# Kernel tuning notes

Hardware: AMD Instinct MI355X
Metric: run time of the kernel (lower is better)

Reference implementation:

```python
import jax, jax.numpy as jnp
import numpy as np

HID = 16
DATA_DIM = 2
B = 2048
T = 64
RTOL, ATOL = 1e-2, 1e-4
SAFETY, FMIN, FMAX = 0.9, 0.2, 10.0
MAX_STEPS = 16  # bounded adaptive-step budget (masked once t reaches T1)
T1 = 1.0
DT0 = 1.0

# Tsit5 (Tsitouras 2011) tableau
_A2 = (0.161,)
_A3 = (-0.008480655492356989, 0.335480655492357)
_A4 = (2.8971530571054935, -6.359448489975075, 4.3622954328695815)
_A5 = (5.325864828439257, -11.748883564062828, 7.4955393428898365, -0.09249506636175525)
_A6 = (5.86145544294642, -12.92096931784711, 8.159367898576159, -0.071584973281401, -0.028269050394068383)
_B5 = (0.09646076681806523, 0.01, 0.4798896504144996, 1.379008574103742, -3.290069515436081, 2.324710524099774)
_BT = (-0.00178001105222577714, -0.0008164344596567469, 0.007880878010261995, -0.1447110071732629, 0.5823571654525552, -0.45808210592918697, 0.015151515151515152)


def setup_inputs() -> dict:
    key = jax.random.key(0)
    ks = jax.random.split(key, 13)
    u = lambda k, shape, fan: jax.random.uniform(k, shape, jnp.float32, -1.0, 1.0) / np.float32(np.sqrt(fan))
    return dict(
        x_seq=jax.random.normal(ks[0], (B, T, DATA_DIM), jnp.float32),
        w1=u(ks[1], (HID, HID), HID), b1=u(ks[2], (HID,), HID),
        w2=u(ks[3], (HID, HID), HID), b2=u(ks[4], (HID,), HID),
        w3=u(ks[5], (HID, HID), HID), b3=u(ks[6], (HID,), HID),
        gru_wih=u(ks[7], (3 * HID, DATA_DIM), DATA_DIM),
        gru_whh=u(ks[8], (3 * HID, HID), HID),
        gru_b=u(ks[9], (3 * HID,), HID),
        gru_bn=u(ks[10], (HID,), HID),
        pred_w=u(ks[11], (1, HID), HID),
        pred_b=u(ks[12], (1,), HID),
    )


def _mlp(y, w1, b1, w2, b2, w3, b3):
    # eqx.nn.MLP(in=16, out=16, width=16, depth=2, activation=tanh): 3 Linear layers
    y = jnp.tanh(y @ w1.T + b1)
    y = jnp.tanh(y @ w2.T + b2)
    return y @ w3.T + b3


def _ode_solve(h0, f):
    """Adaptive Tsit5 + I-controller (diffrax PIDController defaults) from t=0 to t=1.
    Per-sample adaptive step/accept/reject, batched over the leading axis."""
    nB = h0.shape[0]

    def body(state, _):
        y, t, dt = state                      # y:[B,16]  t,dt:[B]
        dt_c = jnp.minimum(dt, T1 - t)        # clip so we never overshoot t1
        d = dt_c[:, None]
        k1 = f(y)
        k2 = f(y + d * (_A2[0] * k1))
        k3 = f(y + d * (_A3[0] * k1 + _A3[1] * k2))
        k4 = f(y + d * (_A4[0] * k1 + _A4[1] * k2 + _A4[2] * k3))
        k5 = f(y + d * (_A5[0] * k1 + _A5[1] * k2 + _A5[2] * k3 + _A5[3] * k4))
        k6 = f(y + d * (_A6[0] * k1 + _A6[1] * k2 + _A6[2] * k3 + _A6[3] * k4 + _A6[4] * k5))
        y_new = y + d * (_B5[0] * k1 + _B5[1] * k2 + _B5[2] * k3 + _B5[3] * k4 + _B5[4] * k5 + _B5[5] * k6)
        k7 = f(y_new)                          # FSAL stage, enters only the error estimate
        err = d * (_BT[0] * k1 + _BT[1] * k2 + _BT[2] * k3 + _BT[3] * k4 + _BT[4] * k5 + _BT[5] * k6 + _BT[6] * k7)
        scale = ATOL + RTOL * jnp.maximum(jnp.abs(y), jnp.abs(y_new))
        err2 = jnp.maximum(jnp.mean((err / scale) ** 2, axis=-1), 1e-16)  # squared RMS norm, [B]
        accept = err2 <= 1.0
        y = jnp.where(accept[:, None], y_new, y)
        t = jnp.where(accept, t + dt_c, t)
        # I-controller: factor = safety * err_norm**(-1/order), order=5
        factor = jnp.clip(SAFETY * err2 ** (-0.1), FMIN, FMAX)
        dt = dt_c * factor
        return (y, t, dt), None

    init = (h0, jnp.zeros((nB,), h0.dtype), jnp.full((nB,), DT0, h0.dtype))
    (y, _, _), _ = jax.lax.scan(body, init, None, length=MAX_STEPS)
    return y


def _gru(x, h, wih, whh, b, bn):
    # eqx.nn.GRUCell math
    ig = x @ wih.T + b
    hg = h @ whh.T
    ir, iz, inn = jnp.split(ig, 3, axis=-1)
    hr, hz, hn = jnp.split(hg, 3, axis=-1)
    r = jax.nn.sigmoid(ir + hr)
    z = jax.nn.sigmoid(iz + hz)
    n = jnp.tanh(inn + r * (hn + bn))
    return n + z * (h - n)


def reference(x_seq, w1, b1, w2, b2, w3, b3, gru_wih, gru_whh, gru_b, gru_bn, pred_w, pred_b):
    f = lambda y: _mlp(y, w1, b1, w2, b2, w3, b3)
    h0 = jnp.zeros((x_seq.shape[0], HID), x_seq.dtype)

    def step(h, x_t):
        h_ev = _ode_solve(h, f)
        h_new = _gru(x_t, h_ev, gru_wih, gru_whh, gru_b, gru_bn)
        return h_new, None

    xs = jnp.swapaxes(x_seq, 0, 1)  # [T, B, D]
    h_final, _ = jax.lax.scan(step, h0, xs)
    return h_final @ pred_w.T + pred_b  # [B, 1]
```

## Files before the change

### kernel.cpp

```cpp
#include <hip/hip_runtime.h>


#define T_STEPS 64
#define NB 2048
#define N_ODE_STEPS 16

#define ROR(x, r) __int_as_float(__builtin_amdgcn_update_dpp( \
    0, __float_as_int(x), 0x120 + (r), 0xF, 0xF, true))

__device__ __forceinline__ float rsum16(float v) {
  v += ROR(v, 8);
  v += ROR(v, 4);
  v += ROR(v, 2);
  v += ROR(v, 1);
  return v;
}

__device__ __forceinline__ float dot16(const float (&w)[16], float y) {
  float a0 = w[0] * y;
  float a1 = w[1] * ROR(y, 1);
  float a2 = w[2] * ROR(y, 2);
  float a3 = w[3] * ROR(y, 3);
  a0 = fmaf(w[4],  ROR(y, 4),  a0);
  a1 = fmaf(w[5],  ROR(y, 5),  a1);
  a2 = fmaf(w[6],  ROR(y, 6),  a2);
  a3 = fmaf(w[7],  ROR(y, 7),  a3);
  a0 = fmaf(w[8],  ROR(y, 8),  a0);
  a1 = fmaf(w[9],  ROR(y, 9),  a1);
  a2 = fmaf(w[10], ROR(y, 10), a2);
  a3 = fmaf(w[11], ROR(y, 11), a3);
  a0 = fmaf(w[12], ROR(y, 12), a0);
  a1 = fmaf(w[13], ROR(y, 13), a1);
  a2 = fmaf(w[14], ROR(y, 14), a2);
  a3 = fmaf(w[15], ROR(y, 15), a3);
  return (a0 + a1) + (a2 + a3);
}

__device__ __forceinline__ float fast_tanh(float x) {
  float e = __builtin_amdgcn_exp2f(x * 2.885390081777927f);
  return fmaf(-2.0f, __builtin_amdgcn_rcpf(e + 1.0f), 1.0f);
}

__device__ __forceinline__ float sigmoid_(float x) {
  float e = __builtin_amdgcn_exp2f(x * -1.4426950408889634f);
  return __builtin_amdgcn_rcpf(1.0f + e);
}

__device__ __forceinline__ float mlp_f(float y,
    const float (&w1r)[16], float b1v,
    const float (&w2r)[16], float b2v,
    const float (&w3r)[16], float b3v) {
  float h1 = fast_tanh(dot16(w1r, y) + b1v);
  float h2 = fast_tanh(dot16(w2r, h1) + b2v);
  return dot16(w3r, h2) + b3v;
}

__global__ __launch_bounds__(64, 1) void odern_kernel(
    const float* __restrict__ x_seq,
    const float* __restrict__ w1, const float* __restrict__ b1,
    const float* __restrict__ w2, const float* __restrict__ b2,
    const float* __restrict__ w3, const float* __restrict__ b3,
    const float* __restrict__ gru_wih, const float* __restrict__ gru_whh,
    const float* __restrict__ gru_b, const float* __restrict__ gru_bn,
    const float* __restrict__ pred_w, const float* __restrict__ pred_b,
    float* __restrict__ out) {
  const int tid = threadIdx.x;
  const int j = tid & 15;
  const int g = tid >> 4;
  const int b = blockIdx.x * 4 + g;

  float w1r[16], w2r[16], w3r[16], whr[16], wzr[16], wnr[16];
#pragma unroll
  for (int r = 0; r < 16; ++r) {
    const int i = (j - r) & 15;
    w1r[r] = w1[j * 16 + i];
    w2r[r] = w2[j * 16 + i];
    w3r[r] = w3[j * 16 + i];
    whr[r] = gru_whh[j * 16 + i];
    wzr[r] = gru_whh[(16 + j) * 16 + i];
    wnr[r] = gru_whh[(32 + j) * 16 + i];
  }
  const float b1v = b1[j], b2v = b2[j], b3v = b3[j];
  const float wih_r0 = gru_wih[j * 2],        wih_r1 = gru_wih[j * 2 + 1];
  const float wih_z0 = gru_wih[(16 + j) * 2], wih_z1 = gru_wih[(16 + j) * 2 + 1];
  const float wih_n0 = gru_wih[(32 + j) * 2], wih_n1 = gru_wih[(32 + j) * 2 + 1];
  const float gb_r = gru_b[j], gb_z = gru_b[16 + j], gb_n = gru_b[32 + j];
  const float bnv = gru_bn[j];
  const float pwv = pred_w[j], pbv = pred_b[0];

  const float* xp = x_seq + (size_t)b * (T_STEPS * 2);

  float h = 0.0f;
#pragma unroll 1
  for (int t = 0; t < T_STEPS; ++t) {
    const float x0 = xp[2 * t];
    const float x1 = xp[2 * t + 1];

    float y = h;
    float tt = 0.0f, dt = 1.0f;
    float k1 = mlp_f(y, w1r, b1v, w2r, b2v, w3r, b3v);
#pragma unroll 1
    for (int s = 0; s < N_ODE_STEPS; ++s) {
      if (__all(tt >= 1.0f)) break;

      const float dt_c = fminf(dt, 1.0f - tt);
      const float d = dt_c;

      float s2 = 0.161f * k1;
      float k2 = mlp_f(fmaf(d, s2, y), w1r, b1v, w2r, b2v, w3r, b3v);

      float s3 = fmaf(0.335480655492357f, k2, -0.008480655492356989f * k1);
      float k3 = mlp_f(fmaf(d, s3, y), w1r, b1v, w2r, b2v, w3r, b3v);

      float s4 = fmaf(4.3622954328695815f, k3,
                 fmaf(-6.359448489975075f, k2, 2.8971530571054935f * k1));
      float k4 = mlp_f(fmaf(d, s4, y), w1r, b1v, w2r, b2v, w3r, b3v);

      float s5 = fmaf(-0.09249506636175525f, k4,
                 fmaf(7.4955393428898365f, k3,
                 fmaf(-11.748883564062828f, k2, 5.325864828439257f * k1)));
      float k5 = mlp_f(fmaf(d, s5, y), w1r, b1v, w2r, b2v, w3r, b3v);

      float s6 = fmaf(-0.028269050394068383f, k5,
                 fmaf(-0.071584973281401f, k4,
                 fmaf(8.159367898576159f, k3,
                 fmaf(-12.92096931784711f, k2, 5.86145544294642f * k1))));
      float k6 = mlp_f(fmaf(d, s6, y), w1r, b1v, w2r, b2v, w3r, b3v);

      float sy = fmaf(2.324710524099774f, k6,
                 fmaf(-3.290069515436081f, k5,
                 fmaf(1.379008574103742f, k4,
                 fmaf(0.4798896504144996f, k3,
                 fmaf(0.01f, k2, 0.09646076681806523f * k1)))));
      float y_new = fmaf(d, sy, y);

      float k7 = mlp_f(y_new, w1r, b1v, w2r, b2v, w3r, b3v);

      float se = fmaf(0.015151515151515152f, k7,
                 fmaf(-0.45808210592918697f, k6,
                 fmaf(0.5823571654525552f, k5,
                 fmaf(-0.1447110071732629f, k4,
                 fmaf(0.007880878010261995f, k3,
                 fmaf(-0.0008164344596567469f, k2, -0.001780011052225777f * k1))))));
      float err = d * se;

      float scale = fmaf(0.01f, fmaxf(fabsf(y), fabsf(y_new)), 0.0001f);
      float r = err * __builtin_amdgcn_rcpf(scale);
      float m = rsum16(r * r) * 0.0625f;
      float err2 = fmaxf(m, 1e-16f);

      const bool acc = err2 <= 1.0f;
      y = acc ? y_new : y;
      tt = acc ? tt + dt_c : tt;
      k1 = acc ? k7 : k1;

      float fac = 0.9f * __builtin_amdgcn_exp2f(-0.1f * __builtin_amdgcn_logf(err2));
      fac = fminf(fmaxf(fac, 0.2f), 10.0f);
      dt = dt_c * fac;
    }

    float hr = dot16(whr, y);
    float hz = dot16(wzr, y);
    float hn = dot16(wnr, y);
    float ir = fmaf(wih_r1, x1, fmaf(wih_r0, x0, gb_r));
    float iz = fmaf(wih_z1, x1, fmaf(wih_z0, x0, gb_z));
    float in_ = fmaf(wih_n1, x1, fmaf(wih_n0, x0, gb_n));
    float rg = sigmoid_(ir + hr);
    float zg = sigmoid_(iz + hz);
    float ng = fast_tanh(fmaf(rg, hn + bnv, in_));
    h = fmaf(zg, y - ng, ng);
  }

  float ps = rsum16(h * pwv);
  if (j == 0) out[b] = ps + pbv;
}

extern "C" void kernel_launch(void* const* d_in, const int* in_sizes, int n_in,
                              void* d_out, int out_size, void* d_ws, size_t ws_size,
                              hipStream_t stream) {
  (void)in_sizes; (void)n_in; (void)out_size; (void)d_ws; (void)ws_size;
  odern_kernel<<<dim3(NB / 4), dim3(64), 0, stream>>>(
      (const float*)d_in[0],
      (const float*)d_in[1], (const float*)d_in[2],
      (const float*)d_in[3], (const float*)d_in[4],
      (const float*)d_in[5], (const float*)d_in[6],
      (const float*)d_in[7], (const float*)d_in[8],
      (const float*)d_in[9], (const float*)d_in[10],
      (const float*)d_in[11], (const float*)d_in[12],
      (float*)d_out);
}
```

Measured before the change: 192.7 us.

## Split each 16-wide matvec across two half-rows using 32 lanes per sample

Each sample now uses 32 lanes instead of 16: each half handles 8 of the 16 input columns, then combines partial sums with a ds_swizzle and a DPP rotate fix-up. This cuts the per-lane FMA and DPP chain length of each dot product, shortening the serial latency of the MLP evaluations. In exchange the grid doubles to 1024 blocks of 2 samples, so total lane work grows and the swizzle adds LDS-crossbar latency.

```diff
diff --git a/kernel.cpp b/kernel.cpp
--- a/kernel.cpp
+++ b/kernel.cpp
@@ -7,6 +7,7 @@
 
 #define ROR(x, r) __int_as_float(__builtin_amdgcn_update_dpp( \
     0, __float_as_int(x), 0x120 + (r), 0xF, 0xF, true))
+#define SWZ18(x) __int_as_float(__builtin_amdgcn_ds_swizzle(__float_as_int(x), 0x601F))
 
 __device__ __forceinline__ float rsum16(float v) {
   v += ROR(v, 8);
@@ -16,24 +17,32 @@
   return v;
 }
 
-__device__ __forceinline__ float dot16(const float (&w)[16], float y) {
-  float a0 = w[0] * y;
-  float a1 = w[1] * ROR(y, 1);
-  float a2 = w[2] * ROR(y, 2);
-  float a3 = w[3] * ROR(y, 3);
-  a0 = fmaf(w[4],  ROR(y, 4),  a0);
-  a1 = fmaf(w[5],  ROR(y, 5),  a1);
-  a2 = fmaf(w[6],  ROR(y, 6),  a2);
-  a3 = fmaf(w[7],  ROR(y, 7),  a3);
-  a0 = fmaf(w[8],  ROR(y, 8),  a0);
-  a1 = fmaf(w[9],  ROR(y, 9),  a1);
-  a2 = fmaf(w[10], ROR(y, 10), a2);
-  a3 = fmaf(w[11], ROR(y, 11), a3);
-  a0 = fmaf(w[12], ROR(y, 12), a0);
-  a1 = fmaf(w[13], ROR(y, 13), a1);
-  a2 = fmaf(w[14], ROR(y, 14), a2);
-  a3 = fmaf(w[15], ROR(y, 15), a3);
-  return (a0 + a1) + (a2 + a3);
+__device__ __forceinline__ void gather8(float y, float (&G)[8]) {
+  G[0] = y;
+  G[1] = ROR(y, 15);
+  G[2] = ROR(y, 14);
+  G[3] = ROR(y, 13);
+  G[4] = ROR(y, 12);
+  G[5] = ROR(y, 11);
+  G[6] = ROR(y, 10);
+  G[7] = ROR(y, 9);
+}
+
+__device__ __forceinline__ float dot8(const float (&w)[8], const float (&G)[8],
+                                      bool isq1, float bias) {
+  float a0 = w[0] * G[0];
+  float a1 = w[1] * G[1];
+  a0 = fmaf(w[2], G[2], a0);
+  a1 = fmaf(w[3], G[3], a1);
+  a0 = fmaf(w[4], G[4], a0);
+  a1 = fmaf(w[5], G[5], a1);
+  a0 = fmaf(w[6], G[6], a0);
+  a1 = fmaf(w[7], G[7], a1);
+  float acc = a0 + a1;
+  float red = acc + SWZ18(acc);
+  float fix = ROR(red, 8);
+  float r = isq1 ? fix : red;
+  return r + bias;
 }
 
 __device__ __forceinline__ float fast_tanh(float x) {
@@ -47,15 +56,21 @@
 }
 
 __device__ __forceinline__ float mlp_f(float y,
-    const float (&w1r)[16], float b1v,
-    const float (&w2r)[16], float b2v,
-    const float (&w3r)[16], float b3v) {
-  float h1 = fast_tanh(dot16(w1r, y) + b1v);
-  float h2 = fast_tanh(dot16(w2r, h1) + b2v);
-  return dot16(w3r, h2) + b3v;
-}
-
-__global__ __launch_bounds__(64, 1) void odern_kernel(
+    const float (&w1p)[8], float b1v,
+    const float (&w2p)[8], float b2v,
+    const float (&w3p)[8], float b3v, bool isq1) {
+  float G[8];
+  gather8(y, G);
+  float h1 = fast_tanh(dot8(w1p, G, isq1, b1v));
+  gather8(h1, G);
+  float h2 = fast_tanh(dot8(w2p, G, isq1, b2v));
+  gather8(h2, G);
+  return dot8(w3p, G, isq1, b3v);
+}
+
+__global__
+__attribute__((amdgpu_flat_work_group_size(64, 64), amdgpu_waves_per_eu(1, 1)))
+void odern_kernel(
     const float* __restrict__ x_seq,
     const float* __restrict__ w1, const float* __restrict__ b1,
     const float* __restrict__ w2, const float* __restrict__ b2,
@@ -66,19 +81,21 @@
     float* __restrict__ out) {
   const int tid = threadIdx.x;
   const int j = tid & 15;
-  const int g = tid >> 4;
-  const int b = blockIdx.x * 4 + g;
-
-  float w1r[16], w2r[16], w3r[16], whr[16], wzr[16], wnr[16];
+  const bool isq1 = (tid & 16) != 0;
+  const int s = tid >> 5;
+  const int b = blockIdx.x * 2 + s;
+  const int R = (tid & 31) >= 16 ? ((j + 8) & 15) : j;
+
+  float w1p[8], w2p[8], w3p[8], whp[8], wzp[8], wnp[8];
 #pragma unroll
-  for (int r = 0; r < 16; ++r) {
-    const int i = (j - r) & 15;
-    w1r[r] = w1[j * 16 + i];
-    w2r[r] = w2[j * 16 + i];
-    w3r[r] = w3[j * 16 + i];
-    whr[r] = gru_whh[j * 16 + i];
-    wzr[r] = gru_whh[(16 + j) * 16 + i];
-    wnr[r] = gru_whh[(32 + j) * 16 + i];
+  for (int c = 0; c < 8; ++c) {
+    const int i = (j + c) & 15;
+    w1p[c] = w1[R * 16 + i];
+    w2p[c] = w2[R * 16 + i];
+    w3p[c] = w3[R * 16 + i];
+    whp[c] = gru_whh[R * 16 + i];
+    wzp[c] = gru_whh[(16 + R) * 16 + i];
+    wnp[c] = gru_whh[(32 + R) * 16 + i];
   }
   const float b1v = b1[j], b2v = b2[j], b3v = b3[j];
   const float wih_r0 = gru_wih[j * 2],        wih_r1 = gru_wih[j * 2 + 1];
@@ -98,34 +115,34 @@
 
     float y = h;
     float tt = 0.0f, dt = 1.0f;
-    float k1 = mlp_f(y, w1r, b1v, w2r, b2v, w3r, b3v);
+    float k1 = mlp_f(y, w1p, b1v, w2p, b2v, w3p, b3v, isq1);
 #pragma unroll 1
-    for (int s = 0; s < N_ODE_STEPS; ++s) {
+    for (int sidx = 0; sidx < N_ODE_STEPS; ++sidx) {
       if (__all(tt >= 1.0f)) break;
 
       const float dt_c = fminf(dt, 1.0f - tt);
       const float d = dt_c;
 
       float s2 = 0.161f * k1;
-      float k2 = mlp_f(fmaf(d, s2, y), w1r, b1v, w2r, b2v, w3r, b3v);
+      float k2 = mlp_f(fmaf(d, s2, y), w1p, b1v, w2p, b2v, w3p, b3v, isq1);
 
       float s3 = fmaf(0.335480655492357f, k2, -0.008480655492356989f * k1);
-      float k3 = mlp_f(fmaf(d, s3, y), w1r, b1v, w2r, b2v, w3r, b3v);
+      float k3 = mlp_f(fmaf(d, s3, y), w1p, b1v, w2p, b2v, w3p, b3v, isq1);
 
       float s4 = fmaf(4.3622954328695815f, k3,
                  fmaf(-6.359448489975075f, k2, 2.8971530571054935f * k1));
-      float k4 = mlp_f(fmaf(d, s4, y), w1r, b1v, w2r, b2v, w3r, b3v);
+      float k4 = mlp_f(fmaf(d, s4, y), w1p, b1v, w2p, b2v, w3p, b3v, isq1);
 
       float s5 = fmaf(-0.09249506636175525f, k4,
                  fmaf(7.4955393428898365f, k3,
                  fmaf(-11.748883564062828f, k2, 5.325864828439257f * k1)));
-      float k5 = mlp_f(fmaf(d, s5, y), w1r, b1v, w2r, b2v, w3r, b3v);
+      float k5 = mlp_f(fmaf(d, s5, y), w1p, b1v, w2p, b2v, w3p, b3v, isq1);
 
       float s6 = fmaf(-0.028269050394068383f, k5,
                  fmaf(-0.071584973281401f, k4,
                  fmaf(8.159367898576159f, k3,
                  fmaf(-12.92096931784711f, k2, 5.86145544294642f * k1))));
-      float k6 = mlp_f(fmaf(d, s6, y), w1r, b1v, w2r, b2v, w3r, b3v);
+      float k6 = mlp_f(fmaf(d, s6, y), w1p, b1v, w2p, b2v, w3p, b3v, isq1);
 
       float sy = fmaf(2.324710524099774f, k6,
                  fmaf(-3.290069515436081f, k5,
@@ -134,7 +151,7 @@
                  fmaf(0.01f, k2, 0.09646076681806523f * k1)))));
       float y_new = fmaf(d, sy, y);
 
-      float k7 = mlp_f(y_new, w1r, b1v, w2r, b2v, w3r, b3v);
+      float k7 = mlp_f(y_new, w1p, b1v, w2p, b2v, w3p, b3v, isq1);
 
       float se = fmaf(0.015151515151515152f, k7,
                  fmaf(-0.45808210592918697f, k6,
@@ -159,27 +176,29 @@
       dt = dt_c * fac;
     }
 
-    float hr = dot16(whr, y);
-    float hz = dot16(wzr, y);
-    float hn = dot16(wnr, y);
     float ir = fmaf(wih_r1, x1, fmaf(wih_r0, x0, gb_r));
     float iz = fmaf(wih_z1, x1, fmaf(wih_z0, x0, gb_z));
     float in_ = fmaf(wih_n1, x1, fmaf(wih_n0, x0, gb_n));
-    float rg = sigmoid_(ir + hr);
-    float zg = sigmoid_(iz + hz);
-    float ng = fast_tanh(fmaf(rg, hn + bnv, in_));
+    float G[8];
+    gather8(y, G);
+    float pre_r = dot8(whp, G, isq1, ir);
+    float pre_z = dot8(wzp, G, isq1, iz);
+    float hnb   = dot8(wnp, G, isq1, bnv);
+    float rg = sigmoid_(pre_r);
+    float zg = sigmoid_(pre_z);
+    float ng = fast_tanh(fmaf(rg, hnb, in_));
     h = fmaf(zg, y - ng, ng);
   }
 
   float ps = rsum16(h * pwv);
-  if (j == 0) out[b] = ps + pbv;
+  if ((tid & 31) == 0) out[b] = ps + pbv;
 }
 
 extern "C" void kernel_launch(void* const* d_in, const int* in_sizes, int n_in,
                               void* d_out, int out_size, void* d_ws, size_t ws_size,
                               hipStream_t stream) {
   (void)in_sizes; (void)n_in; (void)out_size; (void)d_ws; (void)ws_size;
-  odern_kernel<<<dim3(NB / 4), dim3(64), 0, stream>>>(
+  odern_kernel<<<dim3(NB / 2), dim3(64), 0, stream>>>(
       (const float*)d_in[0],
       (const float*)d_in[1], (const float*)d_in[2],
       (const float*)d_in[3], (const float*)d_in[4],
```

Result: slower. 221.3 us (+14.8%).
